# Optimization experiments

Hardware: AMD Instinct MI355X
Metric: run time of the kernel (lower is better)

Reference implementation:

```python
import jax, jax.numpy as jnp
import numpy as np

NUM_HEADS = 16
NUM_KV_HEADS = 4
HEAD_DIM = 128
DIM = 2048
B, S = 2, 2048


def apply_rotary(t, cos, sin):
    # t: [B, S, H, D]; cos/sin: [S, D//2] -> broadcast [1, S, 1, D//2]
    tr = t.reshape(*t.shape[:-1], HEAD_DIM // 2, 2)
    t_r, t_i = tr[..., 0], tr[..., 1]
    c = cos[None, :, None, :]
    s = sin[None, :, None, :]
    o_r = t_r * c - t_i * s
    o_i = t_r * s + t_i * c
    return jnp.stack([o_r, o_i], axis=-1).reshape(t.shape)


def setup_inputs() -> dict:
    key = jax.random.key(0)
    ks = jax.random.split(key, 7)
    sc = 1.0 / np.sqrt(DIM)
    x = jax.random.normal(ks[0], (B, S, DIM), jnp.float32)
    pos = jnp.arange(S, dtype=jnp.float32)[:, None]
    inv_freq = 1.0 / (10000.0 ** (jnp.arange(0, HEAD_DIM, 2, dtype=jnp.float32) / HEAD_DIM))
    ang = pos * inv_freq[None, :]
    freqs_cos = jnp.cos(ang)
    freqs_sin = jnp.sin(ang)
    w_q = jax.random.normal(ks[1], (DIM, NUM_HEADS * HEAD_DIM), jnp.float32) * sc
    w_k = jax.random.normal(ks[2], (DIM, NUM_KV_HEADS * HEAD_DIM), jnp.float32) * sc
    w_v = jax.random.normal(ks[3], (DIM, NUM_KV_HEADS * HEAD_DIM), jnp.float32) * sc
    w_o = jax.random.normal(ks[4], (NUM_HEADS * HEAD_DIM, DIM), jnp.float32) * sc
    return {"x": x, "freqs_cos": freqs_cos, "freqs_sin": freqs_sin,
            "w_q": w_q, "w_k": w_k, "w_v": w_v, "w_o": w_o}


def reference(x, freqs_cos, freqs_sin, w_q, w_k, w_v, w_o):
    b, s, _ = x.shape
    kv_rep = NUM_HEADS // NUM_KV_HEADS
    q = (x @ w_q).reshape(b, s, NUM_HEADS, HEAD_DIM)
    k = (x @ w_k).reshape(b, s, NUM_KV_HEADS, HEAD_DIM)
    v = (x @ w_v).reshape(b, s, NUM_KV_HEADS, HEAD_DIM)
    q = apply_rotary(q, freqs_cos, freqs_sin)
    k = apply_rotary(k, freqs_cos, freqs_sin)
    # GQA: repeat KV heads to match query heads
    k = jnp.repeat(k, kv_rep, axis=2)
    v = jnp.repeat(v, kv_rep, axis=2)
    scores = jnp.einsum('bqhd,bkhd->bhqk', q, k) / np.sqrt(HEAD_DIM)
    causal = jnp.triu(jnp.full((s, s), -jnp.inf, jnp.float32), k=1)
    scores = scores + causal[None, None, :, :]
    attn = jax.nn.softmax(scores, axis=-1)
    out = jnp.einsum('bhqk,bkhd->bqhd', attn, v).reshape(b, s, NUM_HEADS * HEAD_DIM)
    return out @ w_o
```

## Files before the change

### kernel.cpp

```cpp
#include <hip/hip_runtime.h>
#include <stdint.h>

#define DIMSZ 2048
#define NH 16
#define NKV 4
#define HD 128
#define BATCH 2
#define SEQ 2048
#define MROWS (BATCH*SEQ)
#define NQKV (NH*HD + 2*NKV*HD)

typedef unsigned short u16;
typedef float f32x4 __attribute__((ext_vector_type(4)));
typedef short short8 __attribute__((ext_vector_type(8)));
typedef __bf16 bf16x8 __attribute__((ext_vector_type(8)));
typedef unsigned short u16x4 __attribute__((ext_vector_type(4)));
typedef unsigned short u16x8 __attribute__((ext_vector_type(8)));

__device__ __forceinline__ u16 f2bf(float f) {
  __bf16 h = (__bf16)f;
  return __builtin_bit_cast(u16, h);
}

__device__ __forceinline__ float bf2f(u16 h) {
  union { uint32_t u; float f; } v; v.u = ((uint32_t)h) << 16; return v.f;
}

__device__ __forceinline__ void async16(void* lds, const void* g) {
  __builtin_amdgcn_global_load_lds(
      (const __attribute__((address_space(1))) void*)(g),
      (__attribute__((address_space(3))) void*)(lds), 16, 0, 0);
}

__device__ __forceinline__ bf16x8 load_frag(const u16* p) {
  short8 v = *reinterpret_cast<const short8*>(p);
  return __builtin_bit_cast(bf16x8, v);
}

__global__ __launch_bounds__(256) void prep_kernel(const float* __restrict__ x,
                                                   const float* __restrict__ wq,
                                                   const float* __restrict__ wk,
                                                   const float* __restrict__ wv,
                                                   const float* __restrict__ wo,
                                                   u16* __restrict__ xb,
                                                   u16* __restrict__ wtqkv,
                                                   u16* __restrict__ wto) {
  __shared__ float tb[64][65];
  int y = blockIdx.y;
  if (y >= 80) {
    int id = (y - 80) * 32 + blockIdx.x;
    int i = (id * 256 + (int)threadIdx.x) * 4;
    float4 v = *reinterpret_cast<const float4*>(x + i);
    u16x4 o;
    o.x = f2bf(v.x); o.y = f2bf(v.y); o.z = f2bf(v.z); o.w = f2bf(v.w);
    *reinterpret_cast<u16x4*>(xb + i) = o;
    return;
  }
  const float* src; int srcN; u16* dst; int nbase;
  if (y < 32)      { src = wq; srcN = 2048; dst = wtqkv;                        nbase = y * 64; }
  else if (y < 40) { src = wk; srcN = 512;  dst = wtqkv + (size_t)2048 * 2048;  nbase = (y - 32) * 64; }
  else if (y < 48) { src = wv; srcN = 512;  dst = wtqkv + (size_t)2560 * 2048;  nbase = (y - 40) * 64; }
  else             { src = wo; srcN = 2048; dst = wto;                          nbase = (y - 48) * 64; }
  int k0 = blockIdx.x * 64;
  int t = threadIdx.x;
  int lr = t >> 4, lc = (t & 15) * 4;
#pragma unroll
  for (int i = 0; i < 4; ++i) {
    int row = lr + i * 16;
    float4 v = *reinterpret_cast<const float4*>(&src[(size_t)(k0 + row) * srcN + nbase + lc]);
    tb[row][lc] = v.x; tb[row][lc + 1] = v.y; tb[row][lc + 2] = v.z; tb[row][lc + 3] = v.w;
  }
  __syncthreads();
  int n = t >> 3, kg = (t & 7) * 8;
#pragma unroll
  for (int i = 0; i < 2; ++i) {
    int nn = n + i * 32;
    u16x8 o;
#pragma unroll
    for (int j = 0; j < 8; ++j) o[j] = f2bf(tb[kg + j][nn]);
    *reinterpret_cast<u16x8*>(&dst[(size_t)(nbase + nn) * 2048 + k0 + kg]) = o;
  }
}

#define COMPUTE_PAIR(q)                                                              \
  {                                                                                  \
    bf16x8 af[2][2];                                                                 \
    _Pragma("unroll")                                                                \
    for (int m2 = 0; m2 < 2; ++m2)                                                   \
      _Pragma("unroll")                                                              \
      for (int kk = 0; kk < 2; ++kk)                                                 \
        af[m2][kk] = load_frag(&lds[buf][0][wm * 8192 +                              \
            (((q) * 2 + m2) * 16 + l16) * 64 + ((kk * 4 + lg) ^ (l16 & 7)) * 8]);    \
    __builtin_amdgcn_s_setprio(1);                                                   \
    _Pragma("unroll")                                                                \
    for (int m2 = 0; m2 < 2; ++m2)                                                   \
      _Pragma("unroll")                                                              \
      for (int ni = 0; ni < 4; ++ni)                                                 \
        _Pragma("unroll")                                                            \
        for (int kk = 0; kk < 2; ++kk)                                               \
          acc[(q) * 2 + m2][ni] = __builtin_amdgcn_mfma_f32_16x16x32_bf16(           \
              af[m2][kk], bper[ni][kk], acc[(q) * 2 + m2][ni], 0, 0, 0);             \
    __builtin_amdgcn_s_setprio(0);                                                   \
  }

template <bool BF16OUT>
__global__ __launch_bounds__(512, 2) void gemm8p_kernel(const u16* __restrict__ A,
                                                        const u16* __restrict__ BT,
                                                        void* __restrict__ Cp,
                                                        int M, int N, int K, int gx) {
  __shared__ u16 lds[2][2][16384];
  const int tid = threadIdx.x;
  const int wave = tid >> 6, lane = tid & 63;
  const int l16 = lane & 15, lg = lane >> 4;
  const int wm = wave >> 2, wn = wave & 3;
  const int rloc = lane >> 3;
  const int sOff = ((lane & 7) ^ rloc) * 8;
  const int nwg = gridDim.x;
  const int swz = (blockIdx.x & 7) * (nwg >> 3) + (blockIdx.x >> 3);
  const int bm = (swz / gx) * 256, bn = (swz % gx) * 256;

  f32x4 acc[8][4] = {};

  auto stage = [&](int dstbuf, int x, int h, const u16* xp, int xr0, int kk0) {
#pragma unroll
    for (int j = 0; j < 2; ++j) {
      int c = j * 8 + wave;
      async16(&lds[dstbuf][x][h * 8192 + c * 512],
              xp + (size_t)(xr0 + h * 128 + c * 8 + rloc) * K + kk0 + sOff);
    }
  };

  stage(0, 0, 0, A, bm, 0);
  stage(0, 0, 1, A, bm, 0);
  stage(0, 1, 0, BT, bn, 0);
  stage(0, 1, 1, BT, bn, 0);

  const int NT = K >> 6;
  for (int kt = 0; kt < NT; ++kt) {
    const int buf = kt & 1, nbuf = buf ^ 1;
    const int k0n = (kt + 1) << 6;
    const bool pf = (kt + 1 < NT);
    bf16x8 bper[4][2];

    if (pf) {
      stage(nbuf, 0, 0, A, bm, k0n);
      asm volatile("s_waitcnt vmcnt(2)" ::: "memory");
    } else {
      asm volatile("s_waitcnt vmcnt(0)" ::: "memory");
    }
    __builtin_amdgcn_s_barrier();
    __builtin_amdgcn_sched_barrier(0);
#pragma unroll
    for (int ni = 0; ni < 4; ++ni)
#pragma unroll
      for (int kk = 0; kk < 2; ++kk)
        bper[ni][kk] = load_frag(&lds[buf][1][(wn >> 1) * 8192 +
            ((wn & 1) * 64 + ni * 16 + l16) * 64 + ((kk * 4 + lg) ^ (l16 & 7)) * 8]);
    COMPUTE_PAIR(0)
    if (pf) stage(nbuf, 0, 1, A, bm, k0n);
    __builtin_amdgcn_s_barrier();
    __builtin_amdgcn_sched_barrier(0);
    COMPUTE_PAIR(1)
    if (pf) stage(nbuf, 1, 0, BT, bn, k0n);
    __builtin_amdgcn_s_barrier();
    __builtin_amdgcn_sched_barrier(0);
    COMPUTE_PAIR(2)
    if (pf) stage(nbuf, 1, 1, BT, bn, k0n);
    __builtin_amdgcn_s_barrier();
    __builtin_amdgcn_sched_barrier(0);
    COMPUTE_PAIR(3)
    __builtin_amdgcn_s_barrier();
  }

#pragma unroll
  for (int mi = 0; mi < 8; ++mi)
#pragma unroll
    for (int ni = 0; ni < 4; ++ni)
#pragma unroll
      for (int r = 0; r < 4; ++r) {
        size_t idx = (size_t)(bm + wm * 128 + mi * 16 + lg * 4 + r) * N +
                     bn + wn * 64 + ni * 16 + l16;
        if (BF16OUT) ((u16*)Cp)[idx] = f2bf(acc[mi][ni][r]);
        else         ((float*)Cp)[idx] = acc[mi][ni][r];
      }
}

#define COMPUTE_MB(q)                                                                \
  {                                                                                  \
    bf16x8 af[2];                                                                    \
    _Pragma("unroll")                                                                \
    for (int kk = 0; kk < 2; ++kk)                                                   \
      af[kk] = load_frag(&lds2[buf][(wm * 64 + (q) * 16 + l16) * 64 +                \
                                    ((kk * 4 + lg) ^ (l16 & 7)) * 8]);               \
    __builtin_amdgcn_s_setprio(1);                                                   \
    _Pragma("unroll")                                                                \
    for (int ni = 0; ni < 4; ++ni)                                                   \
      _Pragma("unroll")                                                              \
      for (int kk = 0; kk < 2; ++kk)                                                 \
        acc[(q)][ni] = __builtin_amdgcn_mfma_f32_16x16x32_bf16(                      \
            af[kk], bper[ni][kk], acc[(q)][ni], 0, 0, 0);                            \
    __builtin_amdgcn_s_setprio(0);                                                   \
  }

__global__ __launch_bounds__(512, 2) void gemm8p_n128_kernel(const u16* __restrict__ A,
                                                             const u16* __restrict__ BT,
                                                             float* __restrict__ C,
                                                             int M, int N, int K, int gx) {
  __shared__ u16 lds2[2][24576];
  const int tid = threadIdx.x;
  const int wave = tid >> 6, lane = tid & 63;
  const int l16 = lane & 15, lg = lane >> 4;
  const int wm = wave >> 1, wn = wave & 1;
  const int rloc = lane >> 3;
  const int sOff = ((lane & 7) ^ rloc) * 8;
  const int nwg = gridDim.x;
  const int swz = (blockIdx.x & 7) * (nwg >> 3) + (blockIdx.x >> 3);
  const int bm = (swz / gx) * 256, bn = (swz % gx) * 128;

  f32x4 acc[4][4] = {};

  auto stageA = [&](int dstbuf, int h, int kk0) {
#pragma unroll
    for (int j = 0; j < 2; ++j) {
      int c = j * 8 + wave;
      async16(&lds2[dstbuf][h * 8192 + c * 512],
              A + (size_t)(bm + h * 128 + c * 8 + rloc) * K + kk0 + sOff);
    }
  };
  auto stageB = [&](int dstbuf, int kk0) {
#pragma unroll
    for (int j = 0; j < 2; ++j) {
      int c = j * 8 + wave;
      async16(&lds2[dstbuf][16384 + c * 512],
              BT + (size_t)(bn + c * 8 + rloc) * K + kk0 + sOff);
    }
  };

  stageA(0, 0, 0);
  stageA(0, 1, 0);
  stageB(0, 0);

  const int NT = K >> 6;
  for (int kt = 0; kt < NT; ++kt) {
    const int buf = kt & 1, nbuf = buf ^ 1;
    const int k0n = (kt + 1) << 6;
    const bool pf = (kt + 1 < NT);
    bf16x8 bper[4][2];

    if (pf) {
      stageA(nbuf, 0, k0n);
      asm volatile("s_waitcnt vmcnt(2)" ::: "memory");
    } else {
      asm volatile("s_waitcnt vmcnt(0)" ::: "memory");
    }
    __builtin_amdgcn_s_barrier();
    __builtin_amdgcn_sched_barrier(0);
#pragma unroll
    for (int ni = 0; ni < 4; ++ni)
#pragma unroll
      for (int kk = 0; kk < 2; ++kk)
        bper[ni][kk] = load_frag(&lds2[buf][16384 +
            (wn * 64 + ni * 16 + l16) * 64 + ((kk * 4 + lg) ^ (l16 & 7)) * 8]);
    COMPUTE_MB(0)
    if (pf) stageA(nbuf, 1, k0n);
    __builtin_amdgcn_s_barrier();
    __builtin_amdgcn_sched_barrier(0);
    COMPUTE_MB(1)
    if (pf) stageB(nbuf, k0n);
    __builtin_amdgcn_s_barrier();
    __builtin_amdgcn_sched_barrier(0);
    COMPUTE_MB(2)
    __builtin_amdgcn_s_barrier();
    __builtin_amdgcn_sched_barrier(0);
    COMPUTE_MB(3)
    __builtin_amdgcn_s_barrier();
  }

#pragma unroll
  for (int mb = 0; mb < 4; ++mb)
#pragma unroll
    for (int ni = 0; ni < 4; ++ni)
#pragma unroll
      for (int r = 0; r < 4; ++r)
        C[(size_t)(bm + wm * 64 + mb * 16 + lg * 4 + r) * N +
          bn + wn * 64 + ni * 16 + l16] = acc[mb][ni][r];
}

__global__ __launch_bounds__(256) void rv_kernel(const u16* __restrict__ qkv,
                                                 const float* __restrict__ fc,
                                                 const float* __restrict__ fs,
                                                 u16* __restrict__ Kb,
                                                 u16* __restrict__ vt) {
  __shared__ u16 t[32][33];
  int bid = blockIdx.x;
  if (bid < 4096) {
    int kh = bid >> 10;
    int gi = (bid & 1023) * 256 + (int)threadIdx.x;
    int i = gi & 63;
    int tt = gi >> 6;
    int s = tt & (SEQ - 1), b = tt >> 11;
    float c = fc[s * 64 + i], sn = fs[s * 64 + i];
    uint32_t pr = *reinterpret_cast<const uint32_t*>(&qkv[(size_t)tt * NQKV + NH * HD + kh * HD + 2 * i]);
    float tr = bf2f((u16)(pr & 0xffff)), ti = bf2f((u16)(pr >> 16));
    uint32_t w = (uint32_t)f2bf(tr * c - ti * sn) |
                 ((uint32_t)f2bf(tr * sn + ti * c) << 16);
    *reinterpret_cast<uint32_t*>(&Kb[((size_t)(b * NKV + kh) * SEQ + s) * HD + 2 * i]) = w;
    return;
  }
  int id = bid - 4096;
  int bk = id >> 8;
  int rem = id & 255;
  int s0 = (rem >> 2) * 32;
  int d0 = (rem & 3) * 32;
  int b = bk >> 2, kh = bk & 3;
  int tx = threadIdx.x & 31, ty = threadIdx.x >> 5;
#pragma unroll
  for (int i = 0; i < 4; ++i) {
    int row = ty + i * 8;
    t[row][tx] = qkv[(size_t)(b * SEQ + s0 + row) * NQKV + NH * HD + NKV * HD + kh * HD + d0 + tx];
  }
  __syncthreads();
#pragma unroll
  for (int i = 0; i < 4; ++i) {
    int row = ty + i * 8;
    vt[((size_t)(b * NKV + kh) * HD + d0 + row) * SEQ + s0 + tx] = t[tx][row];
  }
}

__global__ __launch_bounds__(256) void attn_kernel(const u16* __restrict__ qkv,
                                                   const float* __restrict__ fc,
                                                   const float* __restrict__ fs,
                                                   const u16* __restrict__ Kc,
                                                   const u16* __restrict__ VT,
                                                   u16* __restrict__ AO) {
  __shared__ u16 Ks[2][64 * 128];
  __shared__ u16 Vs[128 * 64];
  const int bid = blockIdx.x;
  const int qblk = 31 - (bid >> 5);
  const int bh = bid & 31;
  const int b = bh >> 4, h = bh & 15;
  const int kvh = h >> 2;
  const int tid = threadIdx.x, wave = tid >> 6, lane = tid & 63;
  const int l16 = lane & 15, lg = lane >> 4;
  const int qrow0 = qblk * 64 + wave * 16;
  const int rq = qrow0 + l16;

  const u16* Kbase = Kc + (size_t)(b * NKV + kvh) * SEQ * HD;
  const u16* Vbase = VT + (size_t)(b * NKV + kvh) * HD * SEQ;

  bf16x8 onesf;
#pragma unroll
  for (int j = 0; j < 8; ++j) onesf[j] = __builtin_bit_cast(__bf16, (u16)0x3F80);

  int kOff[4], vOff[4], kDst[4], vDst[4];
#pragma unroll
  for (int i = 0; i < 4; ++i) {
    int chunk = i * 4 + wave;
    int krow = chunk * 4 + (lane >> 4);
    kOff[i] = krow * HD + ((lane & 15) ^ (krow & 15)) * 8;
    kDst[i] = chunk * 512;
    int vrow = chunk * 8 + (lane >> 3);
    vOff[i] = vrow * SEQ + ((lane & 7) ^ (vrow & 7)) * 8;
    vDst[i] = chunk * 512;
  }

  const float qs = 0.12751689760098266f;
  const u16* Qrow = qkv + (size_t)(b * SEQ + rq) * NQKV + h * HD;
  const float* fcb = fc + (size_t)rq * 64;
  const float* fsb = fs + (size_t)rq * 64;
  bf16x8 qf[4];
#pragma unroll
  for (int c = 0; c < 4; ++c) {
    bf16x8 raw = load_frag(Qrow + c * 32 + lg * 8);
    float4 cc = *reinterpret_cast<const float4*>(fcb + c * 16 + lg * 4);
    float4 sv = *reinterpret_cast<const float4*>(fsb + c * 16 + lg * 4);
    bf16x8 q;
#pragma unroll
    for (int j = 0; j < 4; ++j) {
      float e = (float)raw[2 * j], od = (float)raw[2 * j + 1];
      float ce = (&cc.x)[j] * qs, se = (&sv.x)[j] * qs;
      q[2 * j]     = (__bf16)(e * ce - od * se);
      q[2 * j + 1] = (__bf16)(e * se + od * ce);
    }
    qf[c] = q;
  }

  f32x4 o[8] = {};
  f32x4 lsum = {};
  float m = -3e38f;

#pragma unroll
  for (int i = 0; i < 4; ++i) async16(&Ks[0][kDst[i]], Kbase + kOff[i]);

  for (int kt = 0; kt <= qblk; ++kt) {
    const int cur = kt & 1;
    asm volatile("s_waitcnt vmcnt(0)" ::: "memory");
    __builtin_amdgcn_s_barrier();
    __builtin_amdgcn_sched_barrier(0);
    {
      const int k0 = kt * 64;
#pragma unroll
      for (int i = 0; i < 4; ++i) async16(&Vs[vDst[i]], Vbase + k0 + vOff[i]);
      if (kt < qblk) {
        const int k0n = (kt + 1) * 64;
#pragma unroll
        for (int i = 0; i < 4; ++i)
          async16(&Ks[cur ^ 1][kDst[i]], Kbase + (size_t)k0n * HD + kOff[i]);
      }
    }

    f32x4 s[4] = {};
    __builtin_amdgcn_s_setprio(1);
#pragma unroll
    for (int cb = 0; cb < 4; ++cb) {
#pragma unroll
      for (int c = 0; c < 4; ++c) {
        bf16x8 kf = load_frag(&Ks[cur][(cb * 16 + l16) * 128 + (((c * 4 + lg) ^ l16) & 15) * 8]);
        s[cb] = __builtin_amdgcn_mfma_f32_16x16x32_bf16(kf, qf[c], s[cb], 0, 0, 0);
      }
    }
    __builtin_amdgcn_s_setprio(0);

    if (kt == qblk) {
      const int k0 = kt * 64;
#pragma unroll
      for (int cb = 0; cb < 4; ++cb) {
#pragma unroll
        for (int r = 0; r < 4; ++r) {
          int key = k0 + cb * 16 + lg * 4 + r;
          if (key > rq) s[cb][r] = -1e30f;
        }
      }
    }

    float v0 = fmaxf(fmaxf(fmaxf(s[0][0], s[0][1]), fmaxf(s[0][2], s[0][3])),
                     fmaxf(fmaxf(s[1][0], s[1][1]), fmaxf(s[1][2], s[1][3])));
    v0 = fmaxf(v0, fmaxf(fmaxf(fmaxf(s[2][0], s[2][1]), fmaxf(s[2][2], s[2][3])),
                         fmaxf(fmaxf(s[3][0], s[3][1]), fmaxf(s[3][2], s[3][3]))));
    v0 = fmaxf(v0, __shfl_xor(v0, 16));
    v0 = fmaxf(v0, __shfl_xor(v0, 32));

    bool need = v0 > m + 8.f;
    if (__any(need)) {
      float newm = fmaxf(m, v0);
      float sc = exp2f(m - newm);
      m = newm;
      float scR[4];
#pragma unroll
      for (int r = 0; r < 4; ++r) scR[r] = __shfl(sc, lg * 4 + r);
#pragma unroll
      for (int r = 0; r < 4; ++r) {
        lsum[r] *= scR[r];
#pragma unroll
        for (int db = 0; db < 8; ++db) o[db][r] *= scR[r];
      }
    }

    if (kt < qblk) { asm volatile("s_waitcnt vmcnt(4)" ::: "memory"); }
    else           { asm volatile("s_waitcnt vmcnt(0)" ::: "memory"); }
    __builtin_amdgcn_s_barrier();
    __builtin_amdgcn_sched_barrier(0);

    u16* Ps = &Ks[cur][wave * 1280];

#pragma unroll
    for (int cb = 0; cb < 2; ++cb) {
      uint32_t lo = (uint32_t)f2bf(exp2f(s[cb][0] - m)) |
                    ((uint32_t)f2bf(exp2f(s[cb][1] - m)) << 16);
      uint32_t hi = (uint32_t)f2bf(exp2f(s[cb][2] - m)) |
                    ((uint32_t)f2bf(exp2f(s[cb][3] - m)) << 16);
      uint64_t w = (uint64_t)lo | ((uint64_t)hi << 32);
      *reinterpret_cast<uint64_t*>(&Ps[l16 * 40 + cb * 16 + lg * 4]) = w;
    }

    {
      bf16x8 pf = load_frag(&Ps[l16 * 40 + lg * 8]);
      __builtin_amdgcn_s_setprio(1);
      lsum = __builtin_amdgcn_mfma_f32_16x16x32_bf16(pf, onesf, lsum, 0, 0, 0);
#pragma unroll
      for (int db = 0; db < 8; ++db) {
        bf16x8 vf = load_frag(&Vs[(db * 16 + l16) * 64 + ((lg) ^ (l16 & 7)) * 8]);
        o[db] = __builtin_amdgcn_mfma_f32_16x16x32_bf16(pf, vf, o[db], 0, 0, 0);
      }
      __builtin_amdgcn_s_setprio(0);
    }

#pragma unroll
    for (int cb = 2; cb < 4; ++cb) {
      uint32_t lo = (uint32_t)f2bf(exp2f(s[cb][0] - m)) |
                    ((uint32_t)f2bf(exp2f(s[cb][1] - m)) << 16);
      uint32_t hi = (uint32_t)f2bf(exp2f(s[cb][2] - m)) |
                    ((uint32_t)f2bf(exp2f(s[cb][3] - m)) << 16);
      uint64_t w = (uint64_t)lo | ((uint64_t)hi << 32);
      *reinterpret_cast<uint64_t*>(&Ps[l16 * 40 + (cb - 2) * 16 + lg * 4]) = w;
    }

    {
      bf16x8 pf = load_frag(&Ps[l16 * 40 + lg * 8]);
      __builtin_amdgcn_s_setprio(1);
      lsum = __builtin_amdgcn_mfma_f32_16x16x32_bf16(pf, onesf, lsum, 0, 0, 0);
#pragma unroll
      for (int db = 0; db < 8; ++db) {
        bf16x8 vf = load_frag(&Vs[(db * 16 + l16) * 64 + ((4 + lg) ^ (l16 & 7)) * 8]);
        o[db] = __builtin_amdgcn_mfma_f32_16x16x32_bf16(pf, vf, o[db], 0, 0, 0);
      }
      __builtin_amdgcn_s_setprio(0);
    }
  }

#pragma unroll
  for (int r = 0; r < 4; ++r) {
    float inv = 1.f / lsum[r];
    int rqo = qrow0 + lg * 4 + r;
    size_t dst = ((size_t)(b * SEQ + rqo) * NH + h) * HD;
#pragma unroll
    for (int db = 0; db < 8; ++db)
      AO[dst + db * 16 + l16] = f2bf(o[db][r] * inv);
  }
}

extern "C" void kernel_launch(void* const* d_in, const int* in_sizes, int n_in,
                              void* d_out, int out_size, void* d_ws, size_t ws_size,
                              hipStream_t stream) {
  (void)in_sizes; (void)n_in; (void)out_size; (void)ws_size;
  const float* x  = (const float*)d_in[0];
  const float* fc = (const float*)d_in[1];
  const float* fs = (const float*)d_in[2];
  const float* wq = (const float*)d_in[3];
  const float* wk = (const float*)d_in[4];
  const float* wv = (const float*)d_in[5];
  const float* wo = (const float*)d_in[6];
  float* out = (float*)d_out;

  char* ws = (char*)d_ws;
  u16*  xb    = (u16*)(ws);
  u16*  wtqkv = (u16*)(ws + 16777216);
  u16*  wto   = (u16*)(ws + 29360128);
  u16*  qkv   = (u16*)(ws + 37748736);
  u16*  Kb    = (u16*)(ws + 62914560);
  u16*  VTb   = (u16*)(ws + 67108864);
  u16*  AOb   = (u16*)(ws + 71303168);

  prep_kernel<<<dim3(32, 336), dim3(256), 0, stream>>>(x, wq, wk, wv, wo, xb, wtqkv, wto);

  gemm8p_kernel<true><<<dim3(192), dim3(512), 0, stream>>>(xb, wtqkv, qkv, MROWS, NQKV, DIMSZ, 12);

  rv_kernel<<<dim3(6144), dim3(256), 0, stream>>>(qkv, fc, fs, Kb, VTb);

  attn_kernel<<<dim3(1024), dim3(256), 0, stream>>>(qkv, fc, fs, Kb, VTb, AOb);

  gemm8p_n128_kernel<<<dim3(256), dim3(512), 0, stream>>>(AOb, wto, out, MROWS, DIMSZ, DIMSZ, 16);
}
```

Before: 186.3 us.

## Double attention query tile to 128 rows per block, halving K/V reloads

Each attention block now processes 128 query rows: each wave handles two 16-row query groups that share the K and V tiles loaded into shared memory. The grid is halved to 512 blocks. The q-tile order is remapped so the first 256 blocks take the heaviest tiles in descending order and the rest take ascending tiles, to balance causal work. This cuts K/V global and LDS traffic per query row but doubles the accumulator registers per thread, which may reduce occupancy. Fewer blocks also means less parallelism and coarser load balancing.

```diff
diff --git a/kernel.cpp b/kernel.cpp
--- a/kernel.cpp
+++ b/kernel.cpp
@@ -336,14 +336,15 @@
   __shared__ u16 Ks[2][64 * 128];
   __shared__ u16 Vs[128 * 64];
   const int bid = blockIdx.x;
-  const int qblk = 31 - (bid >> 5);
+  const int g = bid >> 5;
+  const int qtile = (bid < 256) ? (15 - g) : (g - 8);
   const int bh = bid & 31;
   const int b = bh >> 4, h = bh & 15;
   const int kvh = h >> 2;
   const int tid = threadIdx.x, wave = tid >> 6, lane = tid & 63;
   const int l16 = lane & 15, lg = lane >> 4;
-  const int qrow0 = qblk * 64 + wave * 16;
-  const int rq = qrow0 + l16;
+  const int qrow0 = qtile * 128 + wave * 32;
+  const int nst = 2 * qtile + 2;
 
   const u16* Kbase = Kc + (size_t)(b * NKV + kvh) * SEQ * HD;
   const u16* Vbase = VT + (size_t)(b * NKV + kvh) * HD * SEQ;
@@ -365,43 +366,47 @@
   }
 
   const float qs = 0.12751689760098266f;
-  const u16* Qrow = qkv + (size_t)(b * SEQ + rq) * NQKV + h * HD;
-  const float* fcb = fc + (size_t)rq * 64;
-  const float* fsb = fs + (size_t)rq * 64;
-  bf16x8 qf[4];
-#pragma unroll
-  for (int c = 0; c < 4; ++c) {
-    bf16x8 raw = load_frag(Qrow + c * 32 + lg * 8);
-    float4 cc = *reinterpret_cast<const float4*>(fcb + c * 16 + lg * 4);
-    float4 sv = *reinterpret_cast<const float4*>(fsb + c * 16 + lg * 4);
-    bf16x8 q;
-#pragma unroll
-    for (int j = 0; j < 4; ++j) {
-      float e = (float)raw[2 * j], od = (float)raw[2 * j + 1];
-      float ce = (&cc.x)[j] * qs, se = (&sv.x)[j] * qs;
-      q[2 * j]     = (__bf16)(e * ce - od * se);
-      q[2 * j + 1] = (__bf16)(e * se + od * ce);
-    }
-    qf[c] = q;
-  }
-
-  f32x4 o[8] = {};
-  f32x4 lsum = {};
-  float m = -3e38f;
+  bf16x8 qf[2][4];
+#pragma unroll
+  for (int qg = 0; qg < 2; ++qg) {
+    int rqg = qrow0 + qg * 16 + l16;
+    const u16* Qrow = qkv + (size_t)(b * SEQ + rqg) * NQKV + h * HD;
+    const float* fcb = fc + (size_t)rqg * 64;
+    const float* fsb = fs + (size_t)rqg * 64;
+#pragma unroll
+    for (int c = 0; c < 4; ++c) {
+      bf16x8 raw = load_frag(Qrow + c * 32 + lg * 8);
+      float4 cc = *reinterpret_cast<const float4*>(fcb + c * 16 + lg * 4);
+      float4 sv = *reinterpret_cast<const float4*>(fsb + c * 16 + lg * 4);
+      bf16x8 q;
+#pragma unroll
+      for (int j = 0; j < 4; ++j) {
+        float e = (float)raw[2 * j], od = (float)raw[2 * j + 1];
+        float ce = (&cc.x)[j] * qs, se = (&sv.x)[j] * qs;
+        q[2 * j]     = (__bf16)(e * ce - od * se);
+        q[2 * j + 1] = (__bf16)(e * se + od * ce);
+      }
+      qf[qg][c] = q;
+    }
+  }
+
+  f32x4 o[2][8] = {};
+  f32x4 lsum[2] = {};
+  float m[2] = { -3e38f, -3e38f };
 
 #pragma unroll
   for (int i = 0; i < 4; ++i) async16(&Ks[0][kDst[i]], Kbase + kOff[i]);
 
-  for (int kt = 0; kt <= qblk; ++kt) {
+  for (int kt = 0; kt < nst; ++kt) {
     const int cur = kt & 1;
     asm volatile("s_waitcnt vmcnt(0)" ::: "memory");
     __builtin_amdgcn_s_barrier();
     __builtin_amdgcn_sched_barrier(0);
     {
-      const int k0 = kt * 64;
-#pragma unroll
-      for (int i = 0; i < 4; ++i) async16(&Vs[vDst[i]], Vbase + k0 + vOff[i]);
-      if (kt < qblk) {
+      const int k0s = kt * 64;
+#pragma unroll
+      for (int i = 0; i < 4; ++i) async16(&Vs[vDst[i]], Vbase + k0s + vOff[i]);
+      if (kt + 1 < nst) {
         const int k0n = (kt + 1) * 64;
 #pragma unroll
         for (int i = 0; i < 4; ++i)
@@ -409,114 +414,130 @@
       }
     }
 
-    f32x4 s[4] = {};
+    f32x4 s[2][4] = {};
     __builtin_amdgcn_s_setprio(1);
 #pragma unroll
     for (int cb = 0; cb < 4; ++cb) {
 #pragma unroll
       for (int c = 0; c < 4; ++c) {
         bf16x8 kf = load_frag(&Ks[cur][(cb * 16 + l16) * 128 + (((c * 4 + lg) ^ l16) & 15) * 8]);
-        s[cb] = __builtin_amdgcn_mfma_f32_16x16x32_bf16(kf, qf[c], s[cb], 0, 0, 0);
+        s[0][cb] = __builtin_amdgcn_mfma_f32_16x16x32_bf16(kf, qf[0][c], s[0][cb], 0, 0, 0);
+        s[1][cb] = __builtin_amdgcn_mfma_f32_16x16x32_bf16(kf, qf[1][c], s[1][cb], 0, 0, 0);
       }
     }
     __builtin_amdgcn_s_setprio(0);
 
-    if (kt == qblk) {
-      const int k0 = kt * 64;
-#pragma unroll
-      for (int cb = 0; cb < 4; ++cb) {
+    const int k0 = kt * 64;
+    if (k0 + 63 > qrow0) {
+#pragma unroll
+      for (int qg = 0; qg < 2; ++qg) {
+        int rqg = qrow0 + qg * 16 + l16;
+#pragma unroll
+        for (int cb = 0; cb < 4; ++cb)
+#pragma unroll
+          for (int r = 0; r < 4; ++r) {
+            int key = k0 + cb * 16 + lg * 4 + r;
+            if (key > rqg) s[qg][cb][r] = -1e30f;
+          }
+      }
+    }
+
+#pragma unroll
+    for (int qg = 0; qg < 2; ++qg) {
+      float v0 = fmaxf(fmaxf(fmaxf(s[qg][0][0], s[qg][0][1]), fmaxf(s[qg][0][2], s[qg][0][3])),
+                       fmaxf(fmaxf(s[qg][1][0], s[qg][1][1]), fmaxf(s[qg][1][2], s[qg][1][3])));
+      v0 = fmaxf(v0, fmaxf(fmaxf(fmaxf(s[qg][2][0], s[qg][2][1]), fmaxf(s[qg][2][2], s[qg][2][3])),
+                           fmaxf(fmaxf(s[qg][3][0], s[qg][3][1]), fmaxf(s[qg][3][2], s[qg][3][3]))));
+      v0 = fmaxf(v0, __shfl_xor(v0, 16));
+      v0 = fmaxf(v0, __shfl_xor(v0, 32));
+      bool need = v0 > m[qg] + 8.f;
+      if (__any(need)) {
+        float newm = fmaxf(m[qg], v0);
+        float sc = exp2f(m[qg] - newm);
+        m[qg] = newm;
+        float scR[4];
+#pragma unroll
+        for (int r = 0; r < 4; ++r) scR[r] = __shfl(sc, lg * 4 + r);
 #pragma unroll
         for (int r = 0; r < 4; ++r) {
-          int key = k0 + cb * 16 + lg * 4 + r;
-          if (key > rq) s[cb][r] = -1e30f;
+          lsum[qg][r] *= scR[r];
+#pragma unroll
+          for (int db = 0; db < 8; ++db) o[qg][db][r] *= scR[r];
         }
       }
     }
 
-    float v0 = fmaxf(fmaxf(fmaxf(s[0][0], s[0][1]), fmaxf(s[0][2], s[0][3])),
-                     fmaxf(fmaxf(s[1][0], s[1][1]), fmaxf(s[1][2], s[1][3])));
-    v0 = fmaxf(v0, fmaxf(fmaxf(fmaxf(s[2][0], s[2][1]), fmaxf(s[2][2], s[2][3])),
-                         fmaxf(fmaxf(s[3][0], s[3][1]), fmaxf(s[3][2], s[3][3]))));
-    v0 = fmaxf(v0, __shfl_xor(v0, 16));
-    v0 = fmaxf(v0, __shfl_xor(v0, 32));
-
-    bool need = v0 > m + 8.f;
-    if (__any(need)) {
-      float newm = fmaxf(m, v0);
-      float sc = exp2f(m - newm);
-      m = newm;
-      float scR[4];
-#pragma unroll
-      for (int r = 0; r < 4; ++r) scR[r] = __shfl(sc, lg * 4 + r);
-#pragma unroll
-      for (int r = 0; r < 4; ++r) {
-        lsum[r] *= scR[r];
-#pragma unroll
-        for (int db = 0; db < 8; ++db) o[db][r] *= scR[r];
-      }
-    }
-
-    if (kt < qblk) { asm volatile("s_waitcnt vmcnt(4)" ::: "memory"); }
-    else           { asm volatile("s_waitcnt vmcnt(0)" ::: "memory"); }
+    if (kt + 1 < nst) { asm volatile("s_waitcnt vmcnt(4)" ::: "memory"); }
+    else              { asm volatile("s_waitcnt vmcnt(0)" ::: "memory"); }
     __builtin_amdgcn_s_barrier();
     __builtin_amdgcn_sched_barrier(0);
 
     u16* Ps = &Ks[cur][wave * 1280];
 
 #pragma unroll
-    for (int cb = 0; cb < 2; ++cb) {
-      uint32_t lo = (uint32_t)f2bf(exp2f(s[cb][0] - m)) |
-                    ((uint32_t)f2bf(exp2f(s[cb][1] - m)) << 16);
-      uint32_t hi = (uint32_t)f2bf(exp2f(s[cb][2] - m)) |
-                    ((uint32_t)f2bf(exp2f(s[cb][3] - m)) << 16);
-      uint64_t w = (uint64_t)lo | ((uint64_t)hi << 32);
-      *reinterpret_cast<uint64_t*>(&Ps[l16 * 40 + cb * 16 + lg * 4]) = w;
-    }
-
+    for (int qg = 0; qg < 2; ++qg)
+#pragma unroll
+      for (int cb = 0; cb < 2; ++cb) {
+        uint32_t lo = (uint32_t)f2bf(exp2f(s[qg][cb][0] - m[qg])) |
+                      ((uint32_t)f2bf(exp2f(s[qg][cb][1] - m[qg])) << 16);
+        uint32_t hi = (uint32_t)f2bf(exp2f(s[qg][cb][2] - m[qg])) |
+                      ((uint32_t)f2bf(exp2f(s[qg][cb][3] - m[qg])) << 16);
+        uint64_t w = (uint64_t)lo | ((uint64_t)hi << 32);
+        *reinterpret_cast<uint64_t*>(&Ps[(qg * 16 + l16) * 40 + cb * 16 + lg * 4]) = w;
+      }
     {
-      bf16x8 pf = load_frag(&Ps[l16 * 40 + lg * 8]);
+      bf16x8 pf0 = load_frag(&Ps[l16 * 40 + lg * 8]);
+      bf16x8 pf1 = load_frag(&Ps[(16 + l16) * 40 + lg * 8]);
       __builtin_amdgcn_s_setprio(1);
-      lsum = __builtin_amdgcn_mfma_f32_16x16x32_bf16(pf, onesf, lsum, 0, 0, 0);
+      lsum[0] = __builtin_amdgcn_mfma_f32_16x16x32_bf16(pf0, onesf, lsum[0], 0, 0, 0);
+      lsum[1] = __builtin_amdgcn_mfma_f32_16x16x32_bf16(pf1, onesf, lsum[1], 0, 0, 0);
 #pragma unroll
       for (int db = 0; db < 8; ++db) {
         bf16x8 vf = load_frag(&Vs[(db * 16 + l16) * 64 + ((lg) ^ (l16 & 7)) * 8]);
-        o[db] = __builtin_amdgcn_mfma_f32_16x16x32_bf16(pf, vf, o[db], 0, 0, 0);
+        o[0][db] = __builtin_amdgcn_mfma_f32_16x16x32_bf16(pf0, vf, o[0][db], 0, 0, 0);
+        o[1][db] = __builtin_amdgcn_mfma_f32_16x16x32_bf16(pf1, vf, o[1][db], 0, 0, 0);
       }
       __builtin_amdgcn_s_setprio(0);
     }
 
 #pragma unroll
-    for (int cb = 2; cb < 4; ++cb) {
-      uint32_t lo = (uint32_t)f2bf(exp2f(s[cb][0] - m)) |
-                    ((uint32_t)f2bf(exp2f(s[cb][1] - m)) << 16);
-      uint32_t hi = (uint32_t)f2bf(exp2f(s[cb][2] - m)) |
-                    ((uint32_t)f2bf(exp2f(s[cb][3] - m)) << 16);
-      uint64_t w = (uint64_t)lo | ((uint64_t)hi << 32);
-      *reinterpret_cast<uint64_t*>(&Ps[l16 * 40 + (cb - 2) * 16 + lg * 4]) = w;
-    }
-
+    for (int qg = 0; qg < 2; ++qg)
+#pragma unroll
+      for (int cb = 2; cb < 4; ++cb) {
+        uint32_t lo = (uint32_t)f2bf(exp2f(s[qg][cb][0] - m[qg])) |
+                      ((uint32_t)f2bf(exp2f(s[qg][cb][1] - m[qg])) << 16);
+        uint32_t hi = (uint32_t)f2bf(exp2f(s[qg][cb][2] - m[qg])) |
+                      ((uint32_t)f2bf(exp2f(s[qg][cb][3] - m[qg])) << 16);
+        uint64_t w = (uint64_t)lo | ((uint64_t)hi << 32);
+        *reinterpret_cast<uint64_t*>(&Ps[(qg * 16 + l16) * 40 + (cb - 2) * 16 + lg * 4]) = w;
+      }
     {
-      bf16x8 pf = load_frag(&Ps[l16 * 40 + lg * 8]);
+      bf16x8 pf0 = load_frag(&Ps[l16 * 40 + lg * 8]);
+      bf16x8 pf1 = load_frag(&Ps[(16 + l16) * 40 + lg * 8]);
       __builtin_amdgcn_s_setprio(1);
-      lsum = __builtin_amdgcn_mfma_f32_16x16x32_bf16(pf, onesf, lsum, 0, 0, 0);
+      lsum[0] = __builtin_amdgcn_mfma_f32_16x16x32_bf16(pf0, onesf, lsum[0], 0, 0, 0);
+      lsum[1] = __builtin_amdgcn_mfma_f32_16x16x32_bf16(pf1, onesf, lsum[1], 0, 0, 0);
 #pragma unroll
       for (int db = 0; db < 8; ++db) {
         bf16x8 vf = load_frag(&Vs[(db * 16 + l16) * 64 + ((4 + lg) ^ (l16 & 7)) * 8]);
-        o[db] = __builtin_amdgcn_mfma_f32_16x16x32_bf16(pf, vf, o[db], 0, 0, 0);
+        o[0][db] = __builtin_amdgcn_mfma_f32_16x16x32_bf16(pf0, vf, o[0][db], 0, 0, 0);
+        o[1][db] = __builtin_amdgcn_mfma_f32_16x16x32_bf16(pf1, vf, o[1][db], 0, 0, 0);
       }
       __builtin_amdgcn_s_setprio(0);
     }
   }
 
 #pragma unroll
-  for (int r = 0; r < 4; ++r) {
-    float inv = 1.f / lsum[r];
-    int rqo = qrow0 + lg * 4 + r;
-    size_t dst = ((size_t)(b * SEQ + rqo) * NH + h) * HD;
-#pragma unroll
-    for (int db = 0; db < 8; ++db)
-      AO[dst + db * 16 + l16] = f2bf(o[db][r] * inv);
-  }
+  for (int qg = 0; qg < 2; ++qg)
+#pragma unroll
+    for (int r = 0; r < 4; ++r) {
+      float inv = 1.f / lsum[qg][r];
+      int rqo = qrow0 + qg * 16 + lg * 4 + r;
+      size_t dst = ((size_t)(b * SEQ + rqo) * NH + h) * HD;
+#pragma unroll
+      for (int db = 0; db < 8; ++db)
+        AO[dst + db * 16 + l16] = f2bf(o[qg][db][r] * inv);
+    }
 }
 
 extern "C" void kernel_launch(void* const* d_in, const int* in_sizes, int n_in,
@@ -547,7 +568,7 @@
 
   rv_kernel<<<dim3(6144), dim3(256), 0, stream>>>(qkv, fc, fs, Kb, VTb);
 
-  attn_kernel<<<dim3(1024), dim3(256), 0, stream>>>(qkv, fc, fs, Kb, VTb, AOb);
+  attn_kernel<<<dim3(512), dim3(256), 0, stream>>>(qkv, fc, fs, Kb, VTb, AOb);
 
   gemm8p_n128_kernel<<<dim3(256), dim3(512), 0, stream>>>(AOb, wto, out, MROWS, DIMSZ, DIMSZ, 16);
 }
```

Measured after the change: 229.5 us. 23.2% more time.
